# Kernel optimization log

Measured on AMD Instinct MI355X. Metric: run time of the kernel, lower is better.

The kernel has to match this reference:

```python
import jax, jax.numpy as jnp
import numpy as np

NF = 16
NC = 1
LENGTH = 256
BATCH = 32
W_BI = 0.05
W_L2 = 0.01
BETA = 2.5        # softmax / window sharpness (beta=2.5 in TemporalOperator ctor)
EPSW = 1e-12


def _st(param, target):
    # straight-through: torch clamps param.data in-place under no_grad, so the
    # forward uses the clamped value but grad flows as identity
    return param + jax.lax.stop_gradient(target - param)


def _wmax(v, w, axis=-1):
    # weighted soft max: softmax(beta*v + log w) selection; w==0 entries ignored
    s = jax.nn.softmax(BETA * v + jnp.log(w + EPSW), axis=axis)
    return jnp.sum(s * v, axis=axis)


def _wmin(v, w, axis=-1):
    return -_wmax(-v, w, axis=axis)


def _win_w(t_lo, t_hi, T):
    # soft indicator of the learnable time window [t_lo, t_hi]; (nf,) -> (nf, T)
    j = jnp.arange(T, dtype=t_lo.dtype)
    return (jax.nn.sigmoid(BETA * (j[None, :] - t_lo[:, None]))
            * jax.nn.sigmoid(BETA * (t_hi[:, None] - j[None, :])))


def _forward(x, t1, t2, a, b, p, tvar_temporal, tvar_logical):
    B, T, _ = x.shape
    # --- parameter projections (match the in-place no_grad clamps) ---
    p_c = _st(p, jnp.clip(p, 0.0, 1.0))
    tvt = _st(tvar_temporal, jnp.clip(tvar_temporal, 0.0, 1.0))
    tvl = _st(tvar_logical, jnp.clip(tvar_logical, 0.0, 1.0))
    t1h = jnp.clip(t1, 0.0, T - 1.0)
    t2h = jnp.clip(t2, 0.0, T - 1.0)
    t1h = jnp.where(t1h >= t2h - 1.0, t2h - 1.0, t1h)
    t1c = _st(t1, t1h)
    t2c = _st(t2, t2h)
    # --- predicate: r = a * x[:, :, 0] - b  -> (B, nf, T) ---
    r1p = a[None, :, None] * x[:, None, :, 0] - b[None, :, None]
    # --- temporal op 1 (padding=True): sliding windows over edge-padded signal ---
    r_pad = jnp.concatenate([r1p, jnp.repeat(r1p[..., -1:], T - 1, axis=-1)], axis=-1)
    idx = jnp.arange(T)[:, None] + jnp.arange(T)[None, :]   # (T_out, T_win)
    win = r_pad[:, :, idx]                                   # (B, nf, T, T)
    w1 = _win_w(t1c[0], t2c[0], T)[None, :, None, :]         # (1, nf, 1, T)
    F1 = _wmax(win, w1)
    G1 = _wmin(win, w1)
    r1i = tvt[0][None, :, None] * F1 + (1.0 - tvt[0])[None, :, None] * G1  # (B, nf, T)
    # --- temporal op 2 (padding=False): reduce whole horizon -> (B, nf) ---
    w2 = _win_w(t1c[1], t2c[1], T)[None]                     # (1, nf, T)
    F2 = _wmax(r1i, w2)
    G2 = _wmin(r1i, w2)
    r1 = tvt[1][None, :] * F2 + (1.0 - tvt[1])[None, :] * G2  # (B, nf)
    # --- logical combine over features with weights p[0] ---
    p0 = p_c[0][None, :]
    r = tvl[0] * _wmax(r1, p0) + (1.0 - tvl[0]) * _wmin(r1, p0)  # (B,)
    # --- regularizers ---
    bi = W_BI * (jnp.sum(tvt * (1.0 - tvt)) + jnp.sum(tvl * (1.0 - tvl))
                 + jnp.sum(p_c * (1.0 - p_c)))
    l2 = W_L2 * jnp.sum(p_c ** 2)
    return r, bi + l2


def setup_inputs() -> dict:
    key = jax.random.key(0)
    ks = jax.random.split(key, 8)
    half = LENGTH // 2
    return {
        "x": jax.random.normal(ks[0], (BATCH, LENGTH, 2), jnp.float32),
        "t1": jax.random.uniform(ks[1], (2, NF), jnp.float32, 0.0, float(half)),
        "t2": jax.random.uniform(ks[2], (2, NF), jnp.float32, float(half), float(LENGTH)),
        "a": jax.random.uniform(ks[3], (NF,), jnp.float32),
        "b": jax.random.uniform(ks[4], (NF,), jnp.float32),
        "p": jax.random.uniform(ks[5], (NC, NF), jnp.float32),
        "tvar_temporal": jax.random.uniform(ks[6], (2, NF), jnp.float32),
        "tvar_logical": jax.random.uniform(ks[7], (NC,), jnp.float32),
    }


def reference(x, t1, t2, a, b, p, tvar_temporal, tvar_logical):
    return _forward(x, t1, t2, a, b, p, tvar_temporal, tvar_logical)
```

## Files before the change

### kernel.cpp

```cpp
#include <hip/hip_runtime.h>
#include <math.h>

#define TLEN   256
#define NFEAT  16
#define NBATCH 32
#define BETA   2.5f
#define EPSW   1e-12f
#define W_BI   0.05f
#define W_L2   0.01f
#define L2E    1.4426950408889634f
#define LB     (BETA * L2E)

#if __has_builtin(__builtin_amdgcn_exp2f)
#define EXP2(x) __builtin_amdgcn_exp2f(x)
#else
#define EXP2(x) exp2f(x)
#endif

__device__ inline float sigm(float v) { return 1.f / (1.f + __expf(-v)); }

__device__ inline float wredmax(float v) {
#pragma unroll
    for (int o = 32; o; o >>= 1) v = fmaxf(v, __shfl_xor(v, o));
    return v;
}
__device__ inline float wredmin(float v) {
#pragma unroll
    for (int o = 32; o; o >>= 1) v = fminf(v, __shfl_xor(v, o));
    return v;
}
__device__ inline float wredsum(float v) {
#pragma unroll
    for (int o = 32; o; o >>= 1) v += __shfl_xor(v, o);
    return v;
}

__global__ __launch_bounds__(256) void stage12_kernel(
    const float* __restrict__ x, const float* __restrict__ t1,
    const float* __restrict__ t2, const float* __restrict__ a,
    const float* __restrict__ b, const float* __restrict__ tvt,
    float* __restrict__ r1_out)
{
    const int bf   = blockIdx.x;
    const int bb   = bf >> 4;
    const int f    = bf & 15;
    const int tid  = threadIdx.x;
    const int wave = tid >> 6;
    const int lane = tid & 63;

    __shared__ float4 PQ[256];
    __shared__ float4 PS[257];
    __shared__ float  wpe[256];
    __shared__ float4 wt4[4];
    __shared__ float  redA[4], redB[4], redC[4], redD[4];

    float t2h = fminf(fmaxf(t2[f], 0.f), (float)(TLEN - 1));
    float t1h = fminf(fmaxf(t1[f], 0.f), (float)(TLEN - 1));
    t1h = (t1h >= t2h - 1.f) ? (t2h - 1.f) : t1h;

    const float v   = a[f] * x[(bb * TLEN + tid) * 2] - b[f];
    const float blv = LB * v;

    {
        const float wm = wredmax(v), wn = wredmin(v);
        if (lane == 0) { redA[wave] = wm; redB[wave] = wn; }
    }

    const float jj = (float)tid;
    const float w1 = sigm(BETA * (jj - t1h)) * sigm(BETA * (t2h - jj));
    wpe[tid] = w1 + EPSW;
    __syncthreads();

    const float vmax = fmaxf(fmaxf(redA[0], redA[1]), fmaxf(redA[2], redA[3]));
    const float vmin = fminf(fminf(redB[0], redB[1]), fminf(redB[2], redB[3]));

    const float Ep = EXP2(blv - LB * vmax);
    const float Em = EXP2(LB * vmin - blv);
    const float4 q = make_float4(Ep, Ep * blv, Em, Em * blv);
    PQ[tid] = q;

    float4 sc = q;
#pragma unroll
    for (int off = 1; off < 64; off <<= 1) {
        const float ox = __shfl_up(sc.x, off), oy = __shfl_up(sc.y, off);
        const float oz = __shfl_up(sc.z, off), ow = __shfl_up(sc.w, off);
        if (lane >= off) { sc.x += ox; sc.y += oy; sc.z += oz; sc.w += ow; }
    }
    if (lane == 63) wt4[wave] = sc;
    __syncthreads();

    {
        float ax = 0.f, ay = 0.f, az = 0.f, aw = 0.f;
        for (int w = 0; w < wave; ++w) {
            const float4 t = wt4[w];
            ax += t.x; ay += t.y; az += t.z; aw += t.w;
        }
        PS[tid + 1] = make_float4(sc.x + ax, sc.y + ay, sc.z + az, sc.w + aw);
        if (tid == 0) PS[0] = make_float4(0.f, 0.f, 0.f, 0.f);
    }
    __syncthreads();

    const int it1  = (int)t1h, it2 = (int)t2h;
    const int jbeg = max(0, it1 - 16);
    const int jc0  = it1 + 7;
    int       jc1  = (int)(t2h - 6.f);
    if (jc1 < jc0) jc1 = jc0 - 1;
    const int jend = min(TLEN - 1, it2 + 17);

    const int i = tid;
    const float4 PQ255 = PQ[255];

    float sp, np, sm, nm;
    {
        const int lo = i + jc0, hi = i + jc1;
        const float4 psh = PS[min(hi + 1, 256)];
        const float4 psl = PS[min(lo, 256)];
        const float cf = (float)(max(0, hi - 255) - max(0, lo - 256));
        sp = psh.x - psl.x + cf * PQ255.x;
        np = psh.y - psl.y + cf * PQ255.y;
        sm = psh.z - psl.z + cf * PQ255.z;
        nm = psh.w - psl.w + cf * PQ255.w;
    }

#pragma unroll 4
    for (int j = jbeg; j < jc0; ++j) {
        const float  wj = wpe[j];
        const float4 pq = PQ[min(i + j, 255)];
        sp = fmaf(wj, pq.x, sp); np = fmaf(wj, pq.y, np);
        sm = fmaf(wj, pq.z, sm); nm = fmaf(wj, pq.w, nm);
    }
#pragma unroll 4
    for (int j = jc1 + 1; j <= jend; ++j) {
        const float  wj = wpe[j];
        const float4 pq = PQ[min(i + j, 255)];
        sp = fmaf(wj, pq.x, sp); np = fmaf(wj, pq.y, np);
        sm = fmaf(wj, pq.z, sm); nm = fmaf(wj, pq.w, nm);
    }

    const float F1  = np / sp;
    const float G1  = nm / sm;
    const float tv0 = fminf(fmaxf(tvt[f], 0.f), 1.f);
    const float y   = (tv0 * F1 + (1.f - tv0) * G1) * (1.f / LB);

    float lw2;
    {
        float t2h2 = fminf(fmaxf(t2[NFEAT + f], 0.f), (float)(TLEN - 1));
        float t1h2 = fminf(fmaxf(t1[NFEAT + f], 0.f), (float)(TLEN - 1));
        t1h2 = (t1h2 >= t2h2 - 1.f) ? (t2h2 - 1.f) : t1h2;
        const float w2 = sigm(BETA * (jj - t1h2)) * sigm(BETA * (t2h2 - jj));
        lw2 = __logf(w2 + EPSW);
    }

    {
        const float ym = wredmax(y), yn = wredmin(y);
        if (lane == 0) { redA[wave] = ym; redB[wave] = yn; }
    }
    __syncthreads();
    const float ymax = fmaxf(fmaxf(redA[0], redA[1]), fmaxf(redA[2], redA[3]));
    const float ymin = fminf(fminf(redB[0], redB[1]), fminf(redB[2], redB[3]));

    const float ep2 = EXP2(fmaf(LB, y - ymax, L2E * lw2));
    const float em2 = EXP2(fmaf(LB, ymin - y, L2E * lw2));
    float c0 = wredsum(ep2);
    float c1 = wredsum(ep2 * y);
    float c2 = wredsum(em2);
    float c3 = wredsum(em2 * y);
    __syncthreads();
    if (lane == 0) { redA[wave] = c0; redB[wave] = c1; redC[wave] = c2; redD[wave] = c3; }
    __syncthreads();
    if (tid == 0) {
        const float SP2 = redA[0] + redA[1] + redA[2] + redA[3];
        const float NP2 = redB[0] + redB[1] + redB[2] + redB[3];
        const float SM2 = redC[0] + redC[1] + redC[2] + redC[3];
        const float NM2 = redD[0] + redD[1] + redD[2] + redD[3];
        const float F2 = NP2 / SP2, G2 = NM2 / SM2;
        const float tv1 = fminf(fmaxf(tvt[NFEAT + f], 0.f), 1.f);
        r1_out[bb * NFEAT + f] = tv1 * F2 + (1.f - tv1) * G2;
    }
}

__global__ __launch_bounds__(64) void stage3_kernel(
    const float* __restrict__ r1, const float* __restrict__ p,
    const float* __restrict__ tvt, const float* __restrict__ tvl_in,
    float* __restrict__ out)
{
    const int tid = threadIdx.x;
    const float tvl = fminf(fmaxf(tvl_in[0], 0.f), 1.f);

    if (tid < NBATCH) {
        float vv[NFEAT], lwp[NFEAT];
        float mp = -1e30f, mm = -1e30f;
#pragma unroll
        for (int ff = 0; ff < NFEAT; ++ff) {
            const float pc = fminf(fmaxf(p[ff], 0.f), 1.f);
            const float lwf = __logf(pc + EPSW);
            const float v = r1[tid * NFEAT + ff];
            vv[ff] = v; lwp[ff] = lwf;
            mp = fmaxf(mp, fmaf(BETA, v, lwf));
            mm = fmaxf(mm, fmaf(-BETA, v, lwf));
        }
        float sp = 0.f, np = 0.f, sm = 0.f, nm = 0.f;
#pragma unroll
        for (int ff = 0; ff < NFEAT; ++ff) {
            const float ep = __expf(fmaf(BETA, vv[ff], lwp[ff]) - mp);
            sp += ep; np = fmaf(ep, vv[ff], np);
            const float em = __expf(fmaf(-BETA, vv[ff], lwp[ff]) - mm);
            sm += em; nm = fmaf(em, vv[ff], nm);
        }
        out[tid] = tvl * (np / sp) + (1.f - tvl) * (nm / sm);
    }

    if (tid == 0) {
        float bi = 0.f, l2 = 0.f;
#pragma unroll
        for (int k = 0; k < 2 * NFEAT; ++k) {
            const float t = fminf(fmaxf(tvt[k], 0.f), 1.f);
            bi += t * (1.f - t);
        }
        bi += tvl * (1.f - tvl);
#pragma unroll
        for (int ff = 0; ff < NFEAT; ++ff) {
            const float pc = fminf(fmaxf(p[ff], 0.f), 1.f);
            bi += pc * (1.f - pc);
            l2 = fmaf(pc, pc, l2);
        }
        out[NBATCH] = W_BI * bi + W_L2 * l2;
    }
}

extern "C" void kernel_launch(void* const* d_in, const int* in_sizes, int n_in,
                              void* d_out, int out_size, void* d_ws, size_t ws_size,
                              hipStream_t stream)
{
    const float* x   = (const float*)d_in[0];
    const float* t1  = (const float*)d_in[1];
    const float* t2  = (const float*)d_in[2];
    const float* a   = (const float*)d_in[3];
    const float* b   = (const float*)d_in[4];
    const float* p   = (const float*)d_in[5];
    const float* tvt = (const float*)d_in[6];
    const float* tvl = (const float*)d_in[7];
    float* out = (float*)d_out;
    float* r1  = (float*)d_ws;

    stage12_kernel<<<NBATCH * NFEAT, 256, 0, stream>>>(x, t1, t2, a, b, tvt, r1);
    stage3_kernel<<<1, 64, 0, stream>>>(r1, p, tvt, tvl, out);
}
```

Before: 13.65 us.

## Fuse final reduction into main kernel via last-block atomic counter and split edge loops

Merges the two kernels into one: the last block to finish, detected through an atomic counter in the workspace, performs the batch-level soft max/min and the regularizer. Blocks grow to 512 threads, and the two window-edge FMA loops are split across the two halves, each running a fixed 24-iteration trip over a zero-padded weight array. The goal is to remove one kernel launch and the serial edge-loop latency. In exchange, half the threads sit idle during the scan phases, and the counter relies on an uninitialised workspace word that is decoded modulo 512.

```diff
diff --git a/kernel.cpp b/kernel.cpp
--- a/kernel.cpp
+++ b/kernel.cpp
@@ -18,6 +18,7 @@
 #endif
 
 __device__ inline float sigm(float v) { return 1.f / (1.f + __expf(-v)); }
+__device__ inline float clamp01(float v) { return fminf(fmaxf(v, 0.f), 1.f); }
 
 __device__ inline float wredmax(float v) {
 #pragma unroll
@@ -35,196 +36,214 @@
     return v;
 }
 
-__global__ __launch_bounds__(256) void stage12_kernel(
+__global__ __launch_bounds__(512, 4) void fused_kernel(
     const float* __restrict__ x, const float* __restrict__ t1,
     const float* __restrict__ t2, const float* __restrict__ a,
-    const float* __restrict__ b, const float* __restrict__ tvt,
-    float* __restrict__ r1_out)
+    const float* __restrict__ b, const float* __restrict__ p,
+    const float* __restrict__ tvt, const float* __restrict__ tvl_in,
+    float* __restrict__ r1_out, unsigned* __restrict__ counter,
+    float* __restrict__ out)
 {
     const int bf   = blockIdx.x;
     const int bb   = bf >> 4;
     const int f    = bf & 15;
     const int tid  = threadIdx.x;
+    const int half = tid >> 8;
+    const int i    = tid & 255;
     const int wave = tid >> 6;
     const int lane = tid & 63;
 
     __shared__ float4 PQ[256];
     __shared__ float4 PS[257];
-    __shared__ float  wpe[256];
+    __shared__ float  wpad[320];
+    __shared__ float4 part4[256];
     __shared__ float4 wt4[4];
-    __shared__ float  redA[4], redB[4], redC[4], redD[4];
-
-    float t2h = fminf(fmaxf(t2[f], 0.f), (float)(TLEN - 1));
-    float t1h = fminf(fmaxf(t1[f], 0.f), (float)(TLEN - 1));
+    __shared__ float  redA[4], redB[4];
+    __shared__ int    lastFlag;
+
+    float t2h = fminf(fmaxf(t2[f], 0.f), 255.f);
+    float t1h = fminf(fmaxf(t1[f], 0.f), 255.f);
     t1h = (t1h >= t2h - 1.f) ? (t2h - 1.f) : t1h;
-
-    const float v   = a[f] * x[(bb * TLEN + tid) * 2] - b[f];
-    const float blv = LB * v;
-
-    {
+    const int it1 = (int)t1h, it2 = (int)t2h;
+    const int jL  = it1 - 16;
+    const int jT  = max(it2 - 6, it1 + 8);
+
+    float blv = 0.f;
+    if (half == 0) {
+        const float v = a[f] * x[(bb * TLEN + i) * 2] - b[f];
+        blv = LB * v;
         const float wm = wredmax(v), wn = wredmin(v);
         if (lane == 0) { redA[wave] = wm; redB[wave] = wn; }
-    }
-
-    const float jj = (float)tid;
-    const float w1 = sigm(BETA * (jj - t1h)) * sigm(BETA * (t2h - jj));
-    wpe[tid] = w1 + EPSW;
+        const float jj = (float)i;
+        const float w1 = sigm(BETA * (jj - t1h)) * sigm(BETA * (t2h - jj));
+        wpad[16 + i] = w1 + EPSW;
+    } else {
+        if (i < 16) wpad[i] = 0.f;
+        else if (i < 64) wpad[256 + i] = 0.f;
+    }
     __syncthreads();
 
     const float vmax = fmaxf(fmaxf(redA[0], redA[1]), fmaxf(redA[2], redA[3]));
     const float vmin = fminf(fminf(redB[0], redB[1]), fminf(redB[2], redB[3]));
 
-    const float Ep = EXP2(blv - LB * vmax);
-    const float Em = EXP2(LB * vmin - blv);
-    const float4 q = make_float4(Ep, Ep * blv, Em, Em * blv);
-    PQ[tid] = q;
-
-    float4 sc = q;
-#pragma unroll
-    for (int off = 1; off < 64; off <<= 1) {
-        const float ox = __shfl_up(sc.x, off), oy = __shfl_up(sc.y, off);
-        const float oz = __shfl_up(sc.z, off), ow = __shfl_up(sc.w, off);
-        if (lane >= off) { sc.x += ox; sc.y += oy; sc.z += oz; sc.w += ow; }
-    }
-    if (lane == 63) wt4[wave] = sc;
-    __syncthreads();
-
-    {
+    float4 sc = make_float4(0.f, 0.f, 0.f, 0.f);
+    if (half == 0) {
+        const float Ep = EXP2(blv - LB * vmax);
+        const float Em = EXP2(LB * vmin - blv);
+        const float4 q = make_float4(Ep, Ep * blv, Em, Em * blv);
+        PQ[i] = q;
+        sc = q;
+#pragma unroll
+        for (int off = 1; off < 64; off <<= 1) {
+            const float ox = __shfl_up(sc.x, off), oy = __shfl_up(sc.y, off);
+            const float oz = __shfl_up(sc.z, off), ow = __shfl_up(sc.w, off);
+            if (lane >= off) { sc.x += ox; sc.y += oy; sc.z += oz; sc.w += ow; }
+        }
+        if (lane == 63) wt4[wave] = sc;
+    }
+    __syncthreads();
+
+    if (half == 0) {
         float ax = 0.f, ay = 0.f, az = 0.f, aw = 0.f;
         for (int w = 0; w < wave; ++w) {
             const float4 t = wt4[w];
             ax += t.x; ay += t.y; az += t.z; aw += t.w;
         }
-        PS[tid + 1] = make_float4(sc.x + ax, sc.y + ay, sc.z + az, sc.w + aw);
+        PS[i + 1] = make_float4(sc.x + ax, sc.y + ay, sc.z + az, sc.w + aw);
         if (tid == 0) PS[0] = make_float4(0.f, 0.f, 0.f, 0.f);
     }
     __syncthreads();
 
-    const int it1  = (int)t1h, it2 = (int)t2h;
-    const int jbeg = max(0, it1 - 16);
-    const int jc0  = it1 + 7;
-    int       jc1  = (int)(t2h - 6.f);
-    if (jc1 < jc0) jc1 = jc0 - 1;
-    const int jend = min(TLEN - 1, it2 + 17);
-
-    const int i = tid;
-    const float4 PQ255 = PQ[255];
-
-    float sp, np, sm, nm;
-    {
-        const int lo = i + jc0, hi = i + jc1;
+    float sp = 0.f, np = 0.f, sm = 0.f, nm = 0.f;
+    if (half == 0) {
+        const int lo = i + it1 + 8;
+        const int hi = i + jT - 1;
         const float4 psh = PS[min(hi + 1, 256)];
         const float4 psl = PS[min(lo, 256)];
-        const float cf = (float)(max(0, hi - 255) - max(0, lo - 256));
-        sp = psh.x - psl.x + cf * PQ255.x;
-        np = psh.y - psl.y + cf * PQ255.y;
-        sm = psh.z - psl.z + cf * PQ255.z;
-        nm = psh.w - psl.w + cf * PQ255.w;
-    }
-
-#pragma unroll 4
-    for (int j = jbeg; j < jc0; ++j) {
-        const float  wj = wpe[j];
-        const float4 pq = PQ[min(i + j, 255)];
-        sp = fmaf(wj, pq.x, sp); np = fmaf(wj, pq.y, np);
-        sm = fmaf(wj, pq.z, sm); nm = fmaf(wj, pq.w, nm);
-    }
-#pragma unroll 4
-    for (int j = jc1 + 1; j <= jend; ++j) {
-        const float  wj = wpe[j];
-        const float4 pq = PQ[min(i + j, 255)];
-        sp = fmaf(wj, pq.x, sp); np = fmaf(wj, pq.y, np);
-        sm = fmaf(wj, pq.z, sm); nm = fmaf(wj, pq.w, nm);
-    }
-
-    const float F1  = np / sp;
-    const float G1  = nm / sm;
-    const float tv0 = fminf(fmaxf(tvt[f], 0.f), 1.f);
-    const float y   = (tv0 * F1 + (1.f - tv0) * G1) * (1.f / LB);
-
-    float lw2;
-    {
-        float t2h2 = fminf(fmaxf(t2[NFEAT + f], 0.f), (float)(TLEN - 1));
-        float t1h2 = fminf(fmaxf(t1[NFEAT + f], 0.f), (float)(TLEN - 1));
+        const float4 pqe = PQ[255];
+        const float  cf  = (float)(max(0, hi - 255) - max(0, lo - 256));
+        sp = psh.x - psl.x + cf * pqe.x;
+        np = psh.y - psl.y + cf * pqe.y;
+        sm = psh.z - psl.z + cf * pqe.z;
+        nm = psh.w - psl.w + cf * pqe.w;
+#pragma unroll 8
+        for (int k = 0; k < 24; ++k) {
+            const int j = jL + k;
+            const float wj = wpad[16 + j];
+            const int t = min(max(i + j, 0), 255);
+            const float4 pq = PQ[t];
+            sp = fmaf(wj, pq.x, sp); np = fmaf(wj, pq.y, np);
+            sm = fmaf(wj, pq.z, sm); nm = fmaf(wj, pq.w, nm);
+        }
+    } else {
+#pragma unroll 8
+        for (int k = 0; k < 24; ++k) {
+            const int j = jT + k;
+            const float wj = wpad[16 + j];
+            const int t = min(i + j, 255);
+            const float4 pq = PQ[t];
+            sp = fmaf(wj, pq.x, sp); np = fmaf(wj, pq.y, np);
+            sm = fmaf(wj, pq.z, sm); nm = fmaf(wj, pq.w, nm);
+        }
+        part4[i] = make_float4(sp, np, sm, nm);
+    }
+    __syncthreads();
+
+    float y = 0.f, lw2 = 0.f;
+    if (half == 0) {
+        const float4 pb = part4[i];
+        sp += pb.x; np += pb.y; sm += pb.z; nm += pb.w;
+        const float F1 = np / sp, G1 = nm / sm;
+        const float tv0 = clamp01(tvt[f]);
+        y = (tv0 * F1 + (1.f - tv0) * G1) * (1.f / LB);
+
+        float t2h2 = fminf(fmaxf(t2[NFEAT + f], 0.f), 255.f);
+        float t1h2 = fminf(fmaxf(t1[NFEAT + f], 0.f), 255.f);
         t1h2 = (t1h2 >= t2h2 - 1.f) ? (t2h2 - 1.f) : t1h2;
+        const float jj = (float)i;
         const float w2 = sigm(BETA * (jj - t1h2)) * sigm(BETA * (t2h2 - jj));
         lw2 = __logf(w2 + EPSW);
-    }
-
-    {
+
         const float ym = wredmax(y), yn = wredmin(y);
         if (lane == 0) { redA[wave] = ym; redB[wave] = yn; }
     }
     __syncthreads();
+
     const float ymax = fmaxf(fmaxf(redA[0], redA[1]), fmaxf(redA[2], redA[3]));
     const float ymin = fminf(fminf(redB[0], redB[1]), fminf(redB[2], redB[3]));
 
-    const float ep2 = EXP2(fmaf(LB, y - ymax, L2E * lw2));
-    const float em2 = EXP2(fmaf(LB, ymin - y, L2E * lw2));
-    float c0 = wredsum(ep2);
-    float c1 = wredsum(ep2 * y);
-    float c2 = wredsum(em2);
-    float c3 = wredsum(em2 * y);
-    __syncthreads();
-    if (lane == 0) { redA[wave] = c0; redB[wave] = c1; redC[wave] = c2; redD[wave] = c3; }
-    __syncthreads();
+    float4 c = make_float4(0.f, 0.f, 0.f, 0.f);
+    if (half == 0) {
+        const float ep2 = EXP2(fmaf(LB, y - ymax, L2E * lw2));
+        const float em2 = EXP2(fmaf(LB, ymin - y, L2E * lw2));
+        c.x = wredsum(ep2); c.y = wredsum(ep2 * y);
+        c.z = wredsum(em2); c.w = wredsum(em2 * y);
+    }
+    __syncthreads();
+    if (half == 0 && lane == 0) part4[wave] = c;
+    __syncthreads();
+
     if (tid == 0) {
-        const float SP2 = redA[0] + redA[1] + redA[2] + redA[3];
-        const float NP2 = redB[0] + redB[1] + redB[2] + redB[3];
-        const float SM2 = redC[0] + redC[1] + redC[2] + redC[3];
-        const float NM2 = redD[0] + redD[1] + redD[2] + redD[3];
+        const float4 s0 = part4[0], s1 = part4[1], s2 = part4[2], s3 = part4[3];
+        const float SP2 = s0.x + s1.x + s2.x + s3.x;
+        const float NP2 = s0.y + s1.y + s2.y + s3.y;
+        const float SM2 = s0.z + s1.z + s2.z + s3.z;
+        const float NM2 = s0.w + s1.w + s2.w + s3.w;
         const float F2 = NP2 / SP2, G2 = NM2 / SM2;
-        const float tv1 = fminf(fmaxf(tvt[NFEAT + f], 0.f), 1.f);
-        r1_out[bb * NFEAT + f] = tv1 * F2 + (1.f - tv1) * G2;
-    }
-}
-
-__global__ __launch_bounds__(64) void stage3_kernel(
-    const float* __restrict__ r1, const float* __restrict__ p,
-    const float* __restrict__ tvt, const float* __restrict__ tvl_in,
-    float* __restrict__ out)
-{
-    const int tid = threadIdx.x;
-    const float tvl = fminf(fmaxf(tvl_in[0], 0.f), 1.f);
-
-    if (tid < NBATCH) {
-        float vv[NFEAT], lwp[NFEAT];
-        float mp = -1e30f, mm = -1e30f;
-#pragma unroll
-        for (int ff = 0; ff < NFEAT; ++ff) {
-            const float pc = fminf(fmaxf(p[ff], 0.f), 1.f);
-            const float lwf = __logf(pc + EPSW);
-            const float v = r1[tid * NFEAT + ff];
-            vv[ff] = v; lwp[ff] = lwf;
-            mp = fmaxf(mp, fmaf(BETA, v, lwf));
-            mm = fmaxf(mm, fmaf(-BETA, v, lwf));
-        }
-        float sp = 0.f, np = 0.f, sm = 0.f, nm = 0.f;
-#pragma unroll
-        for (int ff = 0; ff < NFEAT; ++ff) {
-            const float ep = __expf(fmaf(BETA, vv[ff], lwp[ff]) - mp);
-            sp += ep; np = fmaf(ep, vv[ff], np);
-            const float em = __expf(fmaf(-BETA, vv[ff], lwp[ff]) - mm);
-            sm += em; nm = fmaf(em, vv[ff], nm);
-        }
-        out[tid] = tvl * (np / sp) + (1.f - tvl) * (nm / sm);
+        const float tv1 = clamp01(tvt[NFEAT + f]);
+        r1_out[bf] = tv1 * F2 + (1.f - tv1) * G2;
     }
 
     if (tid == 0) {
-        float bi = 0.f, l2 = 0.f;
-#pragma unroll
-        for (int k = 0; k < 2 * NFEAT; ++k) {
-            const float t = fminf(fmaxf(tvt[k], 0.f), 1.f);
-            bi += t * (1.f - t);
-        }
-        bi += tvl * (1.f - tvl);
-#pragma unroll
-        for (int ff = 0; ff < NFEAT; ++ff) {
-            const float pc = fminf(fmaxf(p[ff], 0.f), 1.f);
-            bi += pc * (1.f - pc);
-            l2 = fmaf(pc, pc, l2);
-        }
-        out[NBATCH] = W_BI * bi + W_L2 * l2;
+        __threadfence();
+        const unsigned old = atomicAdd(counter, 1u);
+        lastFlag = ((old & 511u) == 511u) ? 1 : 0;
+    }
+    __syncthreads();
+
+    if (lastFlag) {
+        __threadfence();
+        volatile const float* vr1 = r1_out;
+        const float tvl = clamp01(tvl_in[0]);
+
+        if (tid < NBATCH) {
+            float vv[NFEAT], lwp[NFEAT];
+            float mp = -1e30f, mm = -1e30f;
+#pragma unroll
+            for (int ff = 0; ff < NFEAT; ++ff) {
+                const float pc = clamp01(p[ff]);
+                const float lwf = __logf(pc + EPSW);
+                const float v = vr1[tid * NFEAT + ff];
+                vv[ff] = v; lwp[ff] = lwf;
+                mp = fmaxf(mp, fmaf(BETA, v, lwf));
+                mm = fmaxf(mm, fmaf(-BETA, v, lwf));
+            }
+            float sp3 = 0.f, np3 = 0.f, sm3 = 0.f, nm3 = 0.f;
+#pragma unroll
+            for (int ff = 0; ff < NFEAT; ++ff) {
+                const float ep = __expf(fmaf(BETA, vv[ff], lwp[ff]) - mp);
+                sp3 += ep; np3 = fmaf(ep, vv[ff], np3);
+                const float em = __expf(fmaf(-BETA, vv[ff], lwp[ff]) - mm);
+                sm3 += em; nm3 = fmaf(em, vv[ff], nm3);
+            }
+            out[tid] = tvl * (np3 / sp3) + (1.f - tvl) * (nm3 / sm3);
+        }
+        if (tid == NBATCH) {
+            float bi = 0.f, l2 = 0.f;
+#pragma unroll
+            for (int k = 0; k < 2 * NFEAT; ++k) {
+                const float t = clamp01(tvt[k]);
+                bi += t * (1.f - t);
+            }
+            bi += tvl * (1.f - tvl);
+#pragma unroll
+            for (int ff = 0; ff < NFEAT; ++ff) {
+                const float pc = clamp01(p[ff]);
+                bi += pc * (1.f - pc);
+                l2 = fmaf(pc, pc, l2);
+            }
+            out[NBATCH] = W_BI * bi + W_L2 * l2;
+        }
     }
 }
 
@@ -242,7 +261,8 @@
     const float* tvl = (const float*)d_in[7];
     float* out = (float*)d_out;
     float* r1  = (float*)d_ws;
-
-    stage12_kernel<<<NBATCH * NFEAT, 256, 0, stream>>>(x, t1, t2, a, b, tvt, r1);
-    stage3_kernel<<<1, 64, 0, stream>>>(r1, p, tvt, tvl, out);
-}
+    unsigned* counter = (unsigned*)((char*)d_ws + 4096);
+
+    fused_kernel<<<NBATCH * NFEAT, 512, 0, stream>>>(
+        x, t1, t2, a, b, p, tvt, tvl, r1, counter, out);
+}
```

Result: slower. 23.71 us (+73.7%).
